# Kernel tuning notes

Measured on AMD Instinct MI355X. Metric: run time of the kernel, lower is better.

Reference implementation:

```python
import jax, jax.numpy as jnp
import numpy as np

N = 200000
E = 12800000
G = 1024

def setup_inputs() -> dict:
    key = jax.random.key(0)
    k1, k2, k3 = jax.random.split(key, 3)
    node_pos = jax.random.normal(k1, (N, 2), dtype=jnp.float32)
    edge_index = jax.random.randint(k2, (2, E), 0, N, dtype=jnp.int64)
    batch_ids = jnp.sort(jax.random.randint(k3, (N,), 0, G, dtype=jnp.int64))
    return {"node_pos": node_pos, "edge_index": edge_index,
            "batch_ids": batch_ids, "num_graphs": G}

def reference(node_pos, edge_index, batch_ids, num_graphs):
    # gather edge endpoints: [E, 2]
    start = node_pos[edge_index[0]]
    end = node_pos[edge_index[1]]
    # per-edge loss: (||end - start|| - 1)^2, [E]
    diff = end - start
    eu = jnp.sqrt(jnp.sum(diff * diff, axis=1))
    edge_var = jnp.square(eu - 1.0)
    # scatter-mean by graph id of the edge's source node
    seg = batch_ids[edge_index[0]]
    sums = jax.ops.segment_sum(edge_var, seg, num_segments=num_graphs)
    counts = jax.ops.segment_sum(jnp.ones_like(edge_var), seg, num_segments=num_graphs)
    graph_var = sums / jnp.maximum(counts, 1.0)  # [G]
    # self.reduce = torch.mean over graphs
    return jnp.mean(graph_var)
```

## Files before the change

kernel.cpp:

```cpp
#include <hip/hip_runtime.h>
#include <hip/hip_fp16.h>


typedef int iv4 __attribute__((ext_vector_type(4)));

#define GBINS 1024

__device__ __forceinline__ int find_graph(int v, const int* __restrict__ ss, float scale) {
    int g = (int)((float)v * scale);
    g = min(g, GBINS - 1);
    while (v < ss[g]) --g;
    while (v >= ss[g + 1]) ++g;
    return g;
}

__global__ void prep(const float2* __restrict__ pos, const int* __restrict__ batch,
                     uint32_t* __restrict__ pos16, int* __restrict__ startg, int N) {
    int i = blockIdx.x * blockDim.x + threadIdx.x;
    if (i >= N) return;
    float2 p = pos[i];
    __half2 h; h.x = __float2half_rn(p.x); h.y = __float2half_rn(p.y);
    uint32_t u; __builtin_memcpy(&u, &h, 4);
    pos16[i] = u;
    int b = batch[i];
    if (i == 0) { for (int g = 0; g <= b; ++g) startg[g] = 0; }
    else { int a = batch[i - 1]; for (int g = a + 1; g <= b; ++g) startg[g] = i; }
    if (i == N - 1) { for (int g = b + 1; g <= GBINS; ++g) startg[g] = N; }
}

__global__ __launch_bounds__(512)
void fused_kernel(const int* __restrict__ src, const int* __restrict__ dst,
                  const uint32_t* __restrict__ pos16, const int* __restrict__ startg,
                  float* __restrict__ gsum, uint32_t* __restrict__ gcnt,
                  int E, float scale) {
    __shared__ int ss[GBINS + 1];
    __shared__ float hs[GBINS];
    __shared__ uint32_t hc[GBINS];
    const int tid = threadIdx.x;
    for (int i = tid; i < GBINS + 1; i += 512) ss[i] = startg[i];
    for (int i = tid; i < GBINS; i += 512) { hs[i] = 0.f; hc[i] = 0u; }
    __syncthreads();

    const int g8 = ((E & 3) == 0) ? (E >> 3) : 0;
    const iv4* __restrict__ s4 = (const iv4*)src;
    const iv4* __restrict__ d4 = (const iv4*)dst;
    const int gtid = blockIdx.x * 512 + tid, gstride = gridDim.x * 512;

    for (int i = gtid; i < g8; i += gstride) {
        const iv4 sa = __builtin_nontemporal_load(&s4[2 * i]);
        const iv4 sb = __builtin_nontemporal_load(&s4[2 * i + 1]);
        const iv4 da = __builtin_nontemporal_load(&d4[2 * i]);
        const iv4 db = __builtin_nontemporal_load(&d4[2 * i + 1]);
        int sv[8], dv[8];
        #pragma unroll
        for (int k = 0; k < 4; ++k) { sv[k] = sa[k]; sv[4 + k] = sb[k];
                                      dv[k] = da[k]; dv[4 + k] = db[k]; }
        uint32_t ua[8], ub[8];
        #pragma unroll
        for (int k = 0; k < 8; ++k) { ua[k] = pos16[sv[k]]; ub[k] = pos16[dv[k]]; }
        #pragma unroll
        for (int k = 0; k < 8; ++k) {
            __half2 ha, hb;
            __builtin_memcpy(&ha, &ua[k], 4);
            __builtin_memcpy(&hb, &ub[k], 4);
            const float dx = __half2float(hb.x) - __half2float(ha.x);
            const float dy = __half2float(hb.y) - __half2float(ha.y);
            const float t  = sqrtf(fmaf(dx, dx, dy * dy)) - 1.f;
            const int g = find_graph(sv[k], ss, scale);
            atomicAdd(&hs[g], t * t);
            atomicAdd(&hc[g], 1u);
        }
    }
    for (int e = (g8 << 3) + gtid; e < E; e += gstride) {
        const int s = src[e], d = dst[e];
        uint32_t ua = pos16[s], ub = pos16[d];
        __half2 ha, hb;
        __builtin_memcpy(&ha, &ua, 4);
        __builtin_memcpy(&hb, &ub, 4);
        const float dx = __half2float(hb.x) - __half2float(ha.x);
        const float dy = __half2float(hb.y) - __half2float(ha.y);
        const float t  = sqrtf(fmaf(dx, dx, dy * dy)) - 1.f;
        const int g = find_graph(s, ss, scale);
        atomicAdd(&hs[g], t * t);
        atomicAdd(&hc[g], 1u);
    }

    __syncthreads();
    for (int j = tid; j < GBINS; j += 512) {
        const int g = (j + (blockIdx.x << 3)) & (GBINS - 1);
        const uint32_t c = hc[g];
        if (c) { atomicAdd(&gcnt[g], c); atomicAdd(&gsum[g], hs[g]); }
    }
}

__global__ __launch_bounds__(1024)
void edge_accum_mono(const float2* __restrict__ pos, const int* __restrict__ batch,
                     const int* __restrict__ src, const int* __restrict__ dst,
                     float* __restrict__ gsum, uint32_t* __restrict__ gcnt, int E) {
    __shared__ float ls[GBINS];
    __shared__ uint32_t lc[GBINS];
    for (int i = threadIdx.x; i < GBINS; i += blockDim.x) { ls[i] = 0.f; lc[i] = 0u; }
    __syncthreads();
    const int tid = blockIdx.x * blockDim.x + threadIdx.x;
    const int stride = gridDim.x * blockDim.x;
    for (int i = tid; i < E; i += stride) {
        const int s = src[i], d = dst[i];
        const float2 a = pos[s], b = pos[d];
        const int g = batch[s];
        const float dx = b.x - a.x, dy = b.y - a.y;
        const float t = sqrtf(fmaf(dx, dx, dy * dy)) - 1.f;
        atomicAdd(&ls[g], t * t);
        atomicAdd(&lc[g], 1u);
    }
    __syncthreads();
    for (int g = threadIdx.x; g < GBINS; g += blockDim.x) {
        const uint32_t c = lc[g];
        if (c) { atomicAdd(&gsum[g], ls[g]); atomicAdd(&gcnt[g], c); }
    }
}

__global__ void finalize_kernel(const float* __restrict__ gsum,
                                const uint32_t* __restrict__ gcnt,
                                float* __restrict__ out,
                                const int* __restrict__ nG_ptr) {
    const int G = *nG_ptr;
    float v = 0.f;
    for (int g = threadIdx.x; g < G; g += blockDim.x)
        v += gsum[g] / fmaxf((float)gcnt[g], 1.f);
    __shared__ float w[16];
    for (int off = 32; off; off >>= 1) v += __shfl_down(v, off, 64);
    if ((threadIdx.x & 63) == 0) w[threadIdx.x >> 6] = v;
    __syncthreads();
    if (threadIdx.x == 0) {
        float s = 0.f;
        const int nw = (blockDim.x + 63) >> 6;
        for (int i = 0; i < nw; ++i) s += w[i];
        out[0] = s / (float)G;
    }
}

extern "C" void kernel_launch(void* const* d_in, const int* in_sizes, int n_in,
                              void* d_out, int out_size, void* d_ws, size_t ws_size,
                              hipStream_t stream) {
    const float2* pos   = (const float2*)d_in[0];
    const int*    ei    = (const int*)d_in[1];
    const int*    batch = (const int*)d_in[2];
    const int*    nG    = (const int*)d_in[3];

    const int N = in_sizes[0] / 2;
    const int E = in_sizes[1] / 2;
    const int* src = ei;
    const int* dst = ei + E;

    float*    gsum   = (float*)d_ws;
    uint32_t* gcnt   = (uint32_t*)((char*)d_ws + 4096);
    int*      startg = (int*)((char*)d_ws + 8192);
    uint32_t* pos16  = (uint32_t*)((char*)d_ws + 16384);
    const size_t need = 16384 + (size_t)N * 4;
    const bool fast = (ws_size >= need) && (N >= 1);

    (void)hipMemsetAsync(d_ws, 0, 8192, stream);

    if (fast) {
        const float scale = (float)GBINS / (float)N;
        prep<<<(N + 255) / 256, 256, 0, stream>>>(pos, batch, pos16, startg, N);
        fused_kernel<<<1024, 512, 0, stream>>>(src, dst, pos16, startg, gsum, gcnt, E, scale);
    } else {
        edge_accum_mono<<<512, 1024, 0, stream>>>(pos, batch, src, dst, gsum, gcnt, E);
    }
    finalize_kernel<<<1, 1024, 0, stream>>>(gsum, gcnt, (float*)d_out, nG);
}
```

Before: 257.2 us.

## Bucket edges by source/destination node blocks so gathers hit shared memory

```diff
diff --git a/kernel.cpp b/kernel.cpp
--- a/kernel.cpp
+++ b/kernel.cpp
@@ -3,24 +3,26 @@
 
 
 typedef int iv4 __attribute__((ext_vector_type(4)));
+typedef unsigned int u32;
 
 #define GBINS 1024
-
-__device__ __forceinline__ int find_graph(int v, const int* __restrict__ ss, float scale) {
-    int g = (int)((float)v * scale);
-    g = min(g, GBINS - 1);
-    while (v < ss[g]) --g;
-    while (v >= ss[g + 1]) ++g;
-    return g;
+#define BUK   32
+#define NBUK  1024
+#define CHUNK 4096
+#define MAXD  6400
+#define LSSMX 512
+
+__device__ __forceinline__ u32 divm(u32 x, unsigned long long magic) {
+    return (u32)((x * magic) >> 40);
 }
 
 __global__ void prep(const float2* __restrict__ pos, const int* __restrict__ batch,
-                     uint32_t* __restrict__ pos16, int* __restrict__ startg, int N) {
+                     u32* __restrict__ pos16, int* __restrict__ startg, int N) {
     int i = blockIdx.x * blockDim.x + threadIdx.x;
     if (i >= N) return;
     float2 p = pos[i];
     __half2 h; h.x = __float2half_rn(p.x); h.y = __float2half_rn(p.y);
-    uint32_t u; __builtin_memcpy(&u, &h, 4);
+    u32 u; __builtin_memcpy(&u, &h, 4);
     pos16[i] = u;
     int b = batch[i];
     if (i == 0) { for (int g = 0; g <= b; ++g) startg[g] = 0; }
@@ -29,76 +31,169 @@
 }
 
 __global__ __launch_bounds__(512)
-void fused_kernel(const int* __restrict__ src, const int* __restrict__ dst,
-                  const uint32_t* __restrict__ pos16, const int* __restrict__ startg,
-                  float* __restrict__ gsum, uint32_t* __restrict__ gcnt,
-                  int E, float scale) {
-    __shared__ int ss[GBINS + 1];
-    __shared__ float hs[GBINS];
-    __shared__ uint32_t hc[GBINS];
+void phaseA(const int* __restrict__ src, const int* __restrict__ dst,
+            u32* __restrict__ lists, u32* __restrict__ cursors,
+            int E, u32 dnode, unsigned long long magic, u32 cap) {
+    __shared__ u32 cnt[NBUK];
+    __shared__ u32 lofs[NBUK + 1];
+    __shared__ u32 gbase[NBUK];
+    __shared__ u32 stage[CHUNK];
+    __shared__ u32 wsum[8];
     const int tid = threadIdx.x;
-    for (int i = tid; i < GBINS + 1; i += 512) ss[i] = startg[i];
-    for (int i = tid; i < GBINS; i += 512) { hs[i] = 0.f; hc[i] = 0u; }
-    __syncthreads();
-
-    const int g8 = ((E & 3) == 0) ? (E >> 3) : 0;
-    const iv4* __restrict__ s4 = (const iv4*)src;
-    const iv4* __restrict__ d4 = (const iv4*)dst;
-    const int gtid = blockIdx.x * 512 + tid, gstride = gridDim.x * 512;
-
-    for (int i = gtid; i < g8; i += gstride) {
-        const iv4 sa = __builtin_nontemporal_load(&s4[2 * i]);
-        const iv4 sb = __builtin_nontemporal_load(&s4[2 * i + 1]);
-        const iv4 da = __builtin_nontemporal_load(&d4[2 * i]);
-        const iv4 db = __builtin_nontemporal_load(&d4[2 * i + 1]);
-        int sv[8], dv[8];
+    for (int i = tid; i < NBUK; i += 512) cnt[i] = 0;
+    __syncthreads();
+
+    const int base = blockIdx.x * CHUNK;
+    const bool amok = ((E & 3) == 0);
+    int bid[8]; u32 rank[8], rec[8];
+
+    #pragma unroll
+    for (int h = 0; h < 2; ++h) {
+        const int e0 = base + h * 2048 + 4 * tid;
+        iv4 sv, dv;
+        const bool vec = amok && (e0 + 3 < E);
+        if (vec) {
+            sv = __builtin_nontemporal_load((const iv4*)(src + e0));
+            dv = __builtin_nontemporal_load((const iv4*)(dst + e0));
+        }
         #pragma unroll
-        for (int k = 0; k < 4; ++k) { sv[k] = sa[k]; sv[4 + k] = sb[k];
-                                      dv[k] = da[k]; dv[4 + k] = db[k]; }
-        uint32_t ua[8], ub[8];
+        for (int k = 0; k < 4; ++k) {
+            const int j = h * 4 + k, e = e0 + k;
+            int s, d;
+            if (vec)        { s = sv[k];   d = dv[k]; }
+            else if (e < E) { s = src[e];  d = dst[e]; }
+            else            { bid[j] = -1; continue; }
+            const u32 bs = divm((u32)s, magic), bd = divm((u32)d, magic);
+            const u32 sl = (u32)s - bs * dnode, dl = (u32)d - bd * dnode;
+            bid[j]  = (int)(bs * BUK + bd);
+            rec[j]  = (sl << 13) | dl;
+            rank[j] = atomicAdd(&cnt[bid[j]], 1u);
+        }
+    }
+    __syncthreads();
+
+    const int lane = tid & 63, wave = tid >> 6;
+    const u32 a0 = cnt[2 * tid], a1 = cnt[2 * tid + 1];
+    const u32 s = a0 + a1;
+    u32 x = s;
+    #pragma unroll
+    for (int off = 1; off < 64; off <<= 1) {
+        u32 n = __shfl_up(x, off, 64);
+        if (lane >= off) x += n;
+    }
+    if (lane == 63) wsum[wave] = x;
+    __syncthreads();
+    if (wave == 0 && lane < 8) {
+        u32 w = wsum[lane];
         #pragma unroll
-        for (int k = 0; k < 8; ++k) { ua[k] = pos16[sv[k]]; ub[k] = pos16[dv[k]]; }
+        for (int off = 1; off < 8; off <<= 1) {
+            u32 n = __shfl_up(w, off, 64);
+            if (lane >= off) w += n;
+        }
+        wsum[lane] = w;
+    }
+    __syncthreads();
+    const u32 excl = (wave ? wsum[wave - 1] : 0u) + x - s;
+    lofs[2 * tid] = excl;
+    lofs[2 * tid + 1] = excl + a0;
+    if (tid == 511) lofs[NBUK] = excl + s;
+    for (int b = tid; b < NBUK; b += 512) {
+        const u32 c = cnt[b];
+        gbase[b] = c ? atomicAdd(&cursors[b], c) : 0u;
+    }
+    __syncthreads();
+
+    #pragma unroll
+    for (int j = 0; j < 8; ++j)
+        if (bid[j] >= 0) stage[lofs[bid[j]] + rank[j]] = rec[j];
+    __syncthreads();
+
+    const int total = (int)lofs[NBUK];
+    for (int i = tid; i < total; i += 512) {
+        int b = 0;
         #pragma unroll
-        for (int k = 0; k < 8; ++k) {
-            __half2 ha, hb;
-            __builtin_memcpy(&ha, &ua[k], 4);
-            __builtin_memcpy(&hb, &ub[k], 4);
-            const float dx = __half2float(hb.x) - __half2float(ha.x);
-            const float dy = __half2float(hb.y) - __half2float(ha.y);
-            const float t  = sqrtf(fmaf(dx, dx, dy * dy)) - 1.f;
-            const int g = find_graph(sv[k], ss, scale);
-            atomicAdd(&hs[g], t * t);
-            atomicAdd(&hc[g], 1u);
-        }
-    }
-    for (int e = (g8 << 3) + gtid; e < E; e += gstride) {
-        const int s = src[e], d = dst[e];
-        uint32_t ua = pos16[s], ub = pos16[d];
+        for (int st = 512; st; st >>= 1)
+            if (lofs[b + st] <= (u32)i) b += st;
+        const u32 gpos = gbase[b] + ((u32)i - lofs[b]);
+        if (gpos < cap) lists[(size_t)b * cap + gpos] = stage[i];
+    }
+}
+
+__global__ __launch_bounds__(512)
+void phaseB(const u32* __restrict__ pos16, const int* __restrict__ startg,
+            const u32* __restrict__ lists, const u32* __restrict__ cursors,
+            float* __restrict__ gsum, u32* __restrict__ gcnt,
+            int N, u32 dnode, u32 cap, float scale) {
+    __shared__ u32 spos[MAXD];
+    __shared__ u32 dposA[MAXD];
+    __shared__ int lss[LSSMX + 1];
+    __shared__ float hs[LSSMX];
+    __shared__ u32 hc[LSSMX];
+    __shared__ int shGb, shSpan;
+    const int tid = threadIdx.x;
+    const int p = blockIdx.x, bs = p >> 5, bd = p & (BUK - 1);
+    const int s0 = bs * (int)dnode, d0 = bd * (int)dnode;
+    const int ns = min((int)dnode, N - s0);
+    const int nd = min((int)dnode, N - d0);
+    for (int i = tid; i < ns; i += 512) spos[i]  = pos16[s0 + i];
+    for (int i = tid; i < nd; i += 512) dposA[i] = pos16[d0 + i];
+    if (tid == 0) {
+        int v = s0, g = min((int)((float)v * scale), GBINS - 1);
+        while (v < startg[g]) --g;
+        while (v >= startg[g + 1]) ++g;
+        shGb = g;
+        int v2 = s0 + ns - 1, g2 = min((int)((float)v2 * scale), GBINS - 1);
+        while (v2 < startg[g2]) --g2;
+        while (v2 >= startg[g2 + 1]) ++g2;
+        shSpan = min(g2 - g + 1, LSSMX);
+    }
+    __syncthreads();
+    const int gb = shGb, span = shSpan;
+    for (int j = tid; j < span; j += 512) { lss[j] = max(0, startg[gb + j] - s0); hs[j] = 0.f; hc[j] = 0u; }
+    if (tid == 0) lss[span] = ns;
+    __syncthreads();
+
+    const u32 n = min(cursors[p], cap);
+    const u32* __restrict__ lp = lists + (size_t)p * cap;
+    const iv4* __restrict__ lp4 = (const iv4*)lp;
+    const float jsc = (float)span / (float)ns;
+
+    auto proc = [&](u32 r) {
+        const u32 sl = r >> 13, dl = r & 8191u;
+        const u32 ua = spos[sl], ub = dposA[dl];
         __half2 ha, hb;
         __builtin_memcpy(&ha, &ua, 4);
         __builtin_memcpy(&hb, &ub, 4);
         const float dx = __half2float(hb.x) - __half2float(ha.x);
         const float dy = __half2float(hb.y) - __half2float(ha.y);
         const float t  = sqrtf(fmaf(dx, dx, dy * dy)) - 1.f;
-        const int g = find_graph(s, ss, scale);
-        atomicAdd(&hs[g], t * t);
-        atomicAdd(&hc[g], 1u);
-    }
-
-    __syncthreads();
-    for (int j = tid; j < GBINS; j += 512) {
-        const int g = (j + (blockIdx.x << 3)) & (GBINS - 1);
-        const uint32_t c = hc[g];
-        if (c) { atomicAdd(&gcnt[g], c); atomicAdd(&gsum[g], hs[g]); }
+        int j = min((int)((float)sl * jsc), span - 1);
+        while ((int)sl < lss[j]) --j;
+        while ((int)sl >= lss[j + 1]) ++j;
+        atomicAdd(&hs[j], t * t);
+        atomicAdd(&hc[j], 1u);
+    };
+
+    const u32 nv4 = n >> 2;
+    for (u32 q = tid; q < nv4; q += 512) {
+        const iv4 rv = lp4[q];
+        proc((u32)rv.x); proc((u32)rv.y); proc((u32)rv.z); proc((u32)rv.w);
+    }
+    for (u32 i = (nv4 << 2) + tid; i < n; i += 512) proc(lp[i]);
+
+    __syncthreads();
+    for (int j = tid; j < span; j += 512) {
+        const u32 c = hc[j];
+        if (c) { atomicAdd(&gsum[gb + j], hs[j]); atomicAdd(&gcnt[gb + j], c); }
     }
 }
 
 __global__ __launch_bounds__(1024)
 void edge_accum_mono(const float2* __restrict__ pos, const int* __restrict__ batch,
                      const int* __restrict__ src, const int* __restrict__ dst,
-                     float* __restrict__ gsum, uint32_t* __restrict__ gcnt, int E) {
+                     float* __restrict__ gsum, u32* __restrict__ gcnt, int E) {
     __shared__ float ls[GBINS];
-    __shared__ uint32_t lc[GBINS];
+    __shared__ u32 lc[GBINS];
     for (int i = threadIdx.x; i < GBINS; i += blockDim.x) { ls[i] = 0.f; lc[i] = 0u; }
     __syncthreads();
     const int tid = blockIdx.x * blockDim.x + threadIdx.x;
@@ -114,13 +209,13 @@
     }
     __syncthreads();
     for (int g = threadIdx.x; g < GBINS; g += blockDim.x) {
-        const uint32_t c = lc[g];
+        const u32 c = lc[g];
         if (c) { atomicAdd(&gsum[g], ls[g]); atomicAdd(&gcnt[g], c); }
     }
 }
 
 __global__ void finalize_kernel(const float* __restrict__ gsum,
-                                const uint32_t* __restrict__ gcnt,
+                                const u32* __restrict__ gcnt,
                                 float* __restrict__ out,
                                 const int* __restrict__ nG_ptr) {
     const int G = *nG_ptr;
@@ -152,19 +247,28 @@
     const int* src = ei;
     const int* dst = ei + E;
 
-    float*    gsum   = (float*)d_ws;
-    uint32_t* gcnt   = (uint32_t*)((char*)d_ws + 4096);
-    int*      startg = (int*)((char*)d_ws + 8192);
-    uint32_t* pos16  = (uint32_t*)((char*)d_ws + 16384);
-    const size_t need = 16384 + (size_t)N * 4;
-    const bool fast = (ws_size >= need) && (N >= 1);
-
-    (void)hipMemsetAsync(d_ws, 0, 8192, stream);
+    float* gsum   = (float*)d_ws;
+    u32*   gcnt   = (u32*)((char*)d_ws + 4096);
+    u32*   cursors= (u32*)((char*)d_ws + 8192);
+    int*   startg = (int*)((char*)d_ws + 12288);
+    u32*   pos16  = (u32*)((char*)d_ws + 20480);
+    u32*   lists  = (u32*)((char*)d_ws + (1u << 20));
+    const u32 dnode = (u32)((N + BUK - 1) / BUK);
+    const u32 cap   = ((u32)(E / NBUK) + 1500u + 3u) & ~3u;
+    const size_t need = (1u << 20) + (size_t)NBUK * cap * 4;
+    const bool fast = (dnode <= MAXD) && (ws_size >= need) &&
+                      (20480 + (size_t)N * 4 <= (1u << 20)) && (N < (1 << 22));
+
+    (void)hipMemsetAsync(d_ws, 0, 12288, stream);
 
     if (fast) {
+        const unsigned long long magic = ((1ULL << 40) + dnode - 1) / dnode;
         const float scale = (float)GBINS / (float)N;
         prep<<<(N + 255) / 256, 256, 0, stream>>>(pos, batch, pos16, startg, N);
-        fused_kernel<<<1024, 512, 0, stream>>>(src, dst, pos16, startg, gsum, gcnt, E, scale);
+        phaseA<<<(E + CHUNK - 1) / CHUNK, 512, 0, stream>>>(
+            src, dst, lists, cursors, E, dnode, magic, cap);
+        phaseB<<<NBUK, 512, 0, stream>>>(
+            pos16, startg, lists, cursors, gsum, gcnt, N, dnode, cap, scale);
     } else {
         edge_accum_mono<<<512, 1024, 0, stream>>>(pos, batch, src, dst, gsum, gcnt, E);
     }
```

Measured after the change: 326.0 us. +26.8%, slower.

## Gather fp32 positions directly and fold workspace zeroing into prep kernel

Applied to the files above, without the earlier changes.

```diff
diff --git a/kernel.cpp b/kernel.cpp
--- a/kernel.cpp
+++ b/kernel.cpp
@@ -1,8 +1,8 @@
 #include <hip/hip_runtime.h>
-#include <hip/hip_fp16.h>
 
 
 typedef int iv4 __attribute__((ext_vector_type(4)));
+typedef unsigned int u32;
 
 #define GBINS 1024
 
@@ -14,71 +14,55 @@
     return g;
 }
 
-__global__ void prep(const float2* __restrict__ pos, const int* __restrict__ batch,
-                     uint32_t* __restrict__ pos16, int* __restrict__ startg, int N) {
-    int i = blockIdx.x * blockDim.x + threadIdx.x;
+__global__ void prep(const int* __restrict__ batch, int* __restrict__ startg,
+                     float* __restrict__ gsum, u32* __restrict__ gcnt, int N) {
+    const int i = blockIdx.x * blockDim.x + threadIdx.x;
+    if (i < GBINS) { gsum[i] = 0.f; gcnt[i] = 0u; }
     if (i >= N) return;
-    float2 p = pos[i];
-    __half2 h; h.x = __float2half_rn(p.x); h.y = __float2half_rn(p.y);
-    uint32_t u; __builtin_memcpy(&u, &h, 4);
-    pos16[i] = u;
-    int b = batch[i];
+    const int b = batch[i];
     if (i == 0) { for (int g = 0; g <= b; ++g) startg[g] = 0; }
-    else { int a = batch[i - 1]; for (int g = a + 1; g <= b; ++g) startg[g] = i; }
+    else { const int a = batch[i - 1]; for (int g = a + 1; g <= b; ++g) startg[g] = i; }
     if (i == N - 1) { for (int g = b + 1; g <= GBINS; ++g) startg[g] = N; }
 }
 
 __global__ __launch_bounds__(512)
 void fused_kernel(const int* __restrict__ src, const int* __restrict__ dst,
-                  const uint32_t* __restrict__ pos16, const int* __restrict__ startg,
-                  float* __restrict__ gsum, uint32_t* __restrict__ gcnt,
+                  const float2* __restrict__ pos, const int* __restrict__ startg,
+                  float* __restrict__ gsum, u32* __restrict__ gcnt,
                   int E, float scale) {
     __shared__ int ss[GBINS + 1];
     __shared__ float hs[GBINS];
-    __shared__ uint32_t hc[GBINS];
+    __shared__ u32 hc[GBINS];
     const int tid = threadIdx.x;
     for (int i = tid; i < GBINS + 1; i += 512) ss[i] = startg[i];
     for (int i = tid; i < GBINS; i += 512) { hs[i] = 0.f; hc[i] = 0u; }
     __syncthreads();
 
-    const int g8 = ((E & 3) == 0) ? (E >> 3) : 0;
+    const int ngroups = E >> 2;
     const iv4* __restrict__ s4 = (const iv4*)src;
     const iv4* __restrict__ d4 = (const iv4*)dst;
     const int gtid = blockIdx.x * 512 + tid, gstride = gridDim.x * 512;
 
-    for (int i = gtid; i < g8; i += gstride) {
-        const iv4 sa = __builtin_nontemporal_load(&s4[2 * i]);
-        const iv4 sb = __builtin_nontemporal_load(&s4[2 * i + 1]);
-        const iv4 da = __builtin_nontemporal_load(&d4[2 * i]);
-        const iv4 db = __builtin_nontemporal_load(&d4[2 * i + 1]);
-        int sv[8], dv[8];
+    for (int i = gtid; i < ngroups; i += gstride) {
+        const iv4 sv = __builtin_nontemporal_load(&s4[i]);
+        const iv4 dv = __builtin_nontemporal_load(&d4[i]);
+        float2 pa[4], pb[4];
         #pragma unroll
-        for (int k = 0; k < 4; ++k) { sv[k] = sa[k]; sv[4 + k] = sb[k];
-                                      dv[k] = da[k]; dv[4 + k] = db[k]; }
-        uint32_t ua[8], ub[8];
+        for (int k = 0; k < 4; ++k) { pa[k] = pos[sv[k]]; pb[k] = pos[dv[k]]; }
         #pragma unroll
-        for (int k = 0; k < 8; ++k) { ua[k] = pos16[sv[k]]; ub[k] = pos16[dv[k]]; }
-        #pragma unroll
-        for (int k = 0; k < 8; ++k) {
-            __half2 ha, hb;
-            __builtin_memcpy(&ha, &ua[k], 4);
-            __builtin_memcpy(&hb, &ub[k], 4);
-            const float dx = __half2float(hb.x) - __half2float(ha.x);
-            const float dy = __half2float(hb.y) - __half2float(ha.y);
+        for (int k = 0; k < 4; ++k) {
+            const float dx = pb[k].x - pa[k].x;
+            const float dy = pb[k].y - pa[k].y;
             const float t  = sqrtf(fmaf(dx, dx, dy * dy)) - 1.f;
             const int g = find_graph(sv[k], ss, scale);
             atomicAdd(&hs[g], t * t);
             atomicAdd(&hc[g], 1u);
         }
     }
-    for (int e = (g8 << 3) + gtid; e < E; e += gstride) {
+    for (int e = (ngroups << 2) + gtid; e < E; e += gstride) {
         const int s = src[e], d = dst[e];
-        uint32_t ua = pos16[s], ub = pos16[d];
-        __half2 ha, hb;
-        __builtin_memcpy(&ha, &ua, 4);
-        __builtin_memcpy(&hb, &ub, 4);
-        const float dx = __half2float(hb.x) - __half2float(ha.x);
-        const float dy = __half2float(hb.y) - __half2float(ha.y);
+        const float2 a = pos[s], b = pos[d];
+        const float dx = b.x - a.x, dy = b.y - a.y;
         const float t  = sqrtf(fmaf(dx, dx, dy * dy)) - 1.f;
         const int g = find_graph(s, ss, scale);
         atomicAdd(&hs[g], t * t);
@@ -88,39 +72,13 @@
     __syncthreads();
     for (int j = tid; j < GBINS; j += 512) {
         const int g = (j + (blockIdx.x << 3)) & (GBINS - 1);
-        const uint32_t c = hc[g];
+        const u32 c = hc[g];
         if (c) { atomicAdd(&gcnt[g], c); atomicAdd(&gsum[g], hs[g]); }
     }
 }
 
-__global__ __launch_bounds__(1024)
-void edge_accum_mono(const float2* __restrict__ pos, const int* __restrict__ batch,
-                     const int* __restrict__ src, const int* __restrict__ dst,
-                     float* __restrict__ gsum, uint32_t* __restrict__ gcnt, int E) {
-    __shared__ float ls[GBINS];
-    __shared__ uint32_t lc[GBINS];
-    for (int i = threadIdx.x; i < GBINS; i += blockDim.x) { ls[i] = 0.f; lc[i] = 0u; }
-    __syncthreads();
-    const int tid = blockIdx.x * blockDim.x + threadIdx.x;
-    const int stride = gridDim.x * blockDim.x;
-    for (int i = tid; i < E; i += stride) {
-        const int s = src[i], d = dst[i];
-        const float2 a = pos[s], b = pos[d];
-        const int g = batch[s];
-        const float dx = b.x - a.x, dy = b.y - a.y;
-        const float t = sqrtf(fmaf(dx, dx, dy * dy)) - 1.f;
-        atomicAdd(&ls[g], t * t);
-        atomicAdd(&lc[g], 1u);
-    }
-    __syncthreads();
-    for (int g = threadIdx.x; g < GBINS; g += blockDim.x) {
-        const uint32_t c = lc[g];
-        if (c) { atomicAdd(&gsum[g], ls[g]); atomicAdd(&gcnt[g], c); }
-    }
-}
-
 __global__ void finalize_kernel(const float* __restrict__ gsum,
-                                const uint32_t* __restrict__ gcnt,
+                                const u32* __restrict__ gcnt,
                                 float* __restrict__ out,
                                 const int* __restrict__ nG_ptr) {
     const int G = *nG_ptr;
@@ -152,21 +110,12 @@
     const int* src = ei;
     const int* dst = ei + E;
 
-    float*    gsum   = (float*)d_ws;
-    uint32_t* gcnt   = (uint32_t*)((char*)d_ws + 4096);
-    int*      startg = (int*)((char*)d_ws + 8192);
-    uint32_t* pos16  = (uint32_t*)((char*)d_ws + 16384);
-    const size_t need = 16384 + (size_t)N * 4;
-    const bool fast = (ws_size >= need) && (N >= 1);
+    float* gsum   = (float*)d_ws;
+    u32*   gcnt   = (u32*)((char*)d_ws + 4096);
+    int*   startg = (int*)((char*)d_ws + 8192);
 
-    (void)hipMemsetAsync(d_ws, 0, 8192, stream);
-
-    if (fast) {
-        const float scale = (float)GBINS / (float)N;
-        prep<<<(N + 255) / 256, 256, 0, stream>>>(pos, batch, pos16, startg, N);
-        fused_kernel<<<1024, 512, 0, stream>>>(src, dst, pos16, startg, gsum, gcnt, E, scale);
-    } else {
-        edge_accum_mono<<<512, 1024, 0, stream>>>(pos, batch, src, dst, gsum, gcnt, E);
-    }
+    const float scale = (float)GBINS / (float)N;
+    prep<<<(N + 255) / 256, 256, 0, stream>>>(batch, startg, gsum, gcnt, N);
+    fused_kernel<<<1024, 512, 0, stream>>>(src, dst, pos, startg, gsum, gcnt, E, scale);
     finalize_kernel<<<1, 1024, 0, stream>>>(gsum, gcnt, (float*)d_out, nG);
 }
```

Measured after the change: 253.8 us. About the same (-1.3%).
